# Kernel tuning notes

Measured on AMD Instinct MI355X. Metric: run time of the kernel, lower is better.

Reference implementation:

```python
import jax, jax.numpy as jnp
import numpy as np

B = 8192
HID = [256, 128, 64]
OUT = 5
EPS = 1e-5

# neighbor order for branch i: all other branches in ascending index order
NEIGH = np.array([[j for j in range(8) if j != i] for i in range(8)])  # [8,7]
# adjacency gate (row,col) into A.view(-1,8,8) for branch i, neighbor slot k
# (branch 1 uses a transposed pattern for slots 3..6, exactly as in the source)
_G = [
    [(0,1),(0,2),(0,3),(4,0),(5,0),(6,0),(7,0)],
    [(0,1),(2,1),(3,1),(4,1),(5,1),(6,1),(7,1)],
    [(0,2),(1,2),(3,2),(4,2),(5,2),(6,2),(7,2)],
    [(0,3),(1,3),(2,3),(4,3),(5,3),(6,3),(7,3)],
    [(0,4),(1,4),(2,4),(3,4),(5,4),(6,4),(7,4)],
    [(0,5),(1,5),(2,5),(3,5),(4,5),(6,5),(7,5)],
    [(0,6),(1,6),(2,6),(3,6),(4,6),(5,6),(7,6)],
    [(0,7),(1,7),(2,7),(3,7),(4,7),(5,7),(6,7)],
]
GIDX = np.array([[r * 8 + c for (r, c) in row] for row in _G]).reshape(-1)  # [56]


def setup_inputs() -> dict:
    key = jax.random.key(0)
    ks = iter(jax.random.split(key, 64))
    inp = {}
    inp["state"] = jax.random.normal(next(ks), (B, 3), jnp.float32)
    for i in range(1, 9):
        inp[f"Z{i}"] = jax.random.normal(next(ks), (B, 3), jnp.float32)
    inp["A"] = jax.random.uniform(next(ks), (B, 64), jnp.float32)
    din = 3
    for l, dout in enumerate(HID):
        inp[f"W{l}"] = jax.random.normal(next(ks), (8, din, dout), jnp.float32) * 0.05
        inp[f"b{l}"] = jnp.zeros((8, dout), jnp.float32)
        inp[f"g{l}"] = jnp.ones((8, dout), jnp.float32)
        inp[f"be{l}"] = jnp.zeros((8, dout), jnp.float32)
        inp[f"Wg{l}"] = jax.random.normal(next(ks), (8, 7 * din, 7), jnp.float32) * 0.05
        inp[f"bg{l}"] = jnp.zeros((8, 7), jnp.float32)
        din = dout
    inp["Wout"] = jax.random.normal(next(ks), (8, din, OUT), jnp.float32) * 0.05
    inp["bout"] = jnp.zeros((8, OUT), jnp.float32)
    return inp


def _forward(Z, A, layers, Wout, bout):
    # Z: [B,8,D0], A: [B,64]
    b = Z.shape[0]
    gates = A[:, jnp.asarray(GIDX)].reshape(b, 8, 7)  # [B,8,7]
    neigh = jnp.asarray(NEIGH)
    for (W, bias, g, be, Wg, bg) in layers:
        Zn = Z[:, neigh, :]                                   # [B,8,7,D]
        Zall = Zn.reshape(b, 8, -1)                           # [B,8,7D]
        a = jax.nn.softmax(jnp.einsum('bif,ifo->bio', Zall, Wg) + bg, axis=-1)
        NZ = jnp.einsum('bik,bikd->bid', a * gates, Zn)       # attention-weighted neighbor sum
        h = jnp.einsum('bid,ido->bio', Z + NZ, W) + bias
        mu = h.mean(-1, keepdims=True)
        var = ((h - mu) ** 2).mean(-1, keepdims=True)
        h = (h - mu) / jnp.sqrt(var + EPS) * g + be           # per-branch LayerNorm
        Z = jax.nn.relu(h)
    return jnp.tanh(jnp.einsum('bid,ido->bio', Z, Wout) + bout)  # [B,8,5]


def reference(state, Z1, Z2, Z3, Z4, Z5, Z6, Z7, Z8, A,
              W0, b0, g0, be0, Wg0, bg0,
              W1, b1, g1, be1, Wg1, bg1,
              W2, b2, g2, be2, Wg2, bg2,
              Wout, bout):
    Z = jnp.stack([Z1, Z2, Z3, Z4, Z5, Z6, Z7, Z8], axis=1)  # [B,8,3]
    layers = [(W0, b0, g0, be0, Wg0, bg0),
              (W1, b1, g1, be1, Wg1, bg1),
              (W2, b2, g2, be2, Wg2, bg2)]
    return _forward(Z, A, layers, Wout, bout)
```

## Files before the change

### kernel.cpp

```cpp
#include <hip/hip_runtime.h>
#include <math.h>

typedef _Float16 v8h __attribute__((ext_vector_type(8)));
typedef float    v4f __attribute__((ext_vector_type(4)));

#define NB    32
#define DSTR  264
#define WSTR  68
#define EPSLN 1e-5f

struct KP {
  const float* Z[8];
  const float* A;
  const float *W0, *b0, *g0, *be0, *Wg0, *bg0;
  const float *b1, *g1, *be1, *bg1;
  const float *b2, *g2, *be2, *bg2;
  const float *bout;
  const _Float16 *WgT1, *WgT2, *WT1, *WT2, *WoT, *W0T;
  const float *stats;
  float* out;
};

__device__ __forceinline__ void cvt_one(const float* __restrict__ src, _Float16* __restrict__ dst,
                                        int F, int Osrc, int Opad, int t) {
  const int f  = t % F;
  const int io = t / F;
  const int o  = io % Opad;
  const int i  = io / Opad;
  dst[t] = (o < Osrc) ? (_Float16)src[(i * F + f) * Osrc + o] : (_Float16)0.f;
}

#define E1 114688
#define E2 57344
#define E3 4096
#define E4 262144
#define E5 65536
#define E6 65536
#define NSTAT 136

__global__ void cvt_all(const float* __restrict__ Wg1, const float* __restrict__ Wg2,
                        const float* __restrict__ Wout, const float* __restrict__ W1,
                        const float* __restrict__ W2, const float* __restrict__ W0,
                        const float* __restrict__ b0, _Float16* __restrict__ ws) {
  int t = blockIdx.x * 256 + threadIdx.x;
  if (t < E1) { cvt_one(Wg1, ws, 1792, 7, 8, t); return; }
  t -= E1;
  if (t < E2) { cvt_one(Wg2, ws + E1, 896, 7, 8, t); return; }
  t -= E2;
  if (t < E3) { cvt_one(Wout, ws + E1 + E2, 64, 5, 8, t); return; }
  t -= E3;
  if (t < E4) { cvt_one(W1, ws + E1 + E2 + E3, 256, 128, 128, t); return; }
  t -= E4;
  if (t < E5) { cvt_one(W2, ws + E1 + E2 + E3 + E4, 128, 64, 64, t); return; }
  t -= E5;
  if (t < E6) {
    const int k = t & 31;
    const int o = (t >> 5) & 255;
    const int i = t >> 13;
    ws[E1 + E2 + E3 + E4 + E5 + t] = (k < 3) ? (_Float16)W0[(i * 3 + k) * 256 + o] : (_Float16)0.f;
    return;
  }
  t -= E6;
  if (t < NSTAT * 64) {
    float* sf = (float*)(ws + E1 + E2 + E3 + E4 + E5 + E6);
    const int stat = t >> 6, lane = t & 63;
    const int i = stat / 17, j = stat % 17;
    float v = 0.f;
    #pragma unroll
    for (int c = 0; c < 4; ++c) {
      const int o = lane + c * 64;
      float e;
      if (j < 3)        e = W0[(i * 3 + j) * 256 + o];
      else if (j == 3)  e = b0[i * 256 + o];
      else if (j < 13) {
        const int a = (j - 4) / 3, bb = (j - 4) % 3;
        e = W0[(i * 3 + a) * 256 + o] * W0[(i * 3 + bb) * 256 + o];
      } else if (j < 16) {
        const int d = j - 13;
        e = W0[(i * 3 + d) * 256 + o] * b0[i * 256 + o];
      } else {
        const float x = b0[i * 256 + o]; e = x * x;
      }
      v += e;
    }
    #pragma unroll
    for (int mk = 1; mk < 64; mk <<= 1) v += __shfl_xor(v, mk, 64);
    if (lane == 0) sf[stat] = v * (1.f / 256.f);
  }
}

template<int D, int O, int NPRE>
__device__ __forceinline__ void mfma_layer(
    _Float16* __restrict__ zh, float* __restrict__ wbuf, const float* __restrict__ gbuf,
    const v8h* gpre,
    const _Float16* __restrict__ WgT, const float* __restrict__ bg,
    const _Float16* __restrict__ WT, const float* __restrict__ bias,
    const float* __restrict__ g, const float* __restrict__ be,
    const _Float16* __restrict__ preBase, int preStride, v8h* pre,
    int i, int q, int r)
{
  constexpr int KS = D / 32;
  constexpr int NT = O / 16;

  const _Float16* WgB = WgT + (size_t)(i * 8 + r) * (7 * D) + q * 8;
  const _Float16* WB  = WT  + (size_t)(i * O + r) * D + q * 8;

  v8h dbf[NT];
  #pragma unroll
  for (int n = 0; n < NT; ++n) dbf[n] = *(const v8h*)(WB + (size_t)n * 16 * D);

  v8h gbf[7];
  #pragma unroll
  for (int nb = 0; nb < 7; ++nb) gbf[nb] = gpre[nb];

  v4f ca[2][2];
  #pragma unroll
  for (int mt = 0; mt < 2; ++mt)
    #pragma unroll
    for (int c = 0; c < 2; ++c) ca[mt][c] = (v4f){0.f,0.f,0.f,0.f};

  #pragma unroll
  for (int ks = 0; ks < KS; ++ks) {
    const int d0 = ks * 32 + q * 8;
    v8h gbn[7];
    if (ks + 1 < KS) {
      #pragma unroll
      for (int nb = 0; nb < 7; ++nb)
        gbn[nb] = *(const v8h*)(WgB + nb * D + (ks + 1) * 32);
    }
    #pragma unroll
    for (int nb = 0; nb < 7; ++nb) {
      const int nk = nb + (nb >= i);
      const v8h af0 = *(const v8h*)(zh + (nk * NB + r) * DSTR + d0);
      const v8h af1 = *(const v8h*)(zh + (nk * NB + 16 + r) * DSTR + d0);
      ca[0][nb & 1] = __builtin_amdgcn_mfma_f32_16x16x32_f16(af0, gbf[nb], ca[0][nb & 1], 0, 0, 0);
      ca[1][nb & 1] = __builtin_amdgcn_mfma_f32_16x16x32_f16(af1, gbf[nb], ca[1][nb & 1], 0, 0, 0);
    }
    if (ks + 1 < KS) {
      #pragma unroll
      for (int nb = 0; nb < 7; ++nb) gbf[nb] = gbn[nb];
    }
  }
  const v4f gacc[2] = { ca[0][0] + ca[0][1], ca[1][0] + ca[1][1] };

  const float bgv = (r < 7) ? bg[i * 7 + r] : 0.f;
  #pragma unroll
  for (int mt = 0; mt < 2; ++mt) {
    #pragma unroll
    for (int reg = 0; reg < 4; ++reg) {
      const float v = gacc[mt][reg] + bgv;
      float m = (r < 7) ? v : -3.0e38f;
      #pragma unroll
      for (int mk = 1; mk < 16; mk <<= 1) m = fmaxf(m, __shfl_xor(m, mk, 16));
      const float e = (r < 7) ? __expf(v - m) : 0.f;
      float s = e;
      #pragma unroll
      for (int mk = 1; mk < 16; mk <<= 1) s += __shfl_xor(s, mk, 16);
      const int b = mt * 16 + q * 4 + reg;
      if (r < 7) wbuf[b * WSTR + i * 8 + r] = (e / s) * gbuf[b * WSTR + i * 8 + r];
    }
  }

  v4f acc[2][NT];
  #pragma unroll
  for (int mt = 0; mt < 2; ++mt)
    #pragma unroll
    for (int n = 0; n < NT; ++n) acc[mt][n] = (v4f){0.f,0.f,0.f,0.f};

  _Float16 wh[2][7];
  #pragma unroll
  for (int mt = 0; mt < 2; ++mt)
    #pragma unroll
    for (int nb = 0; nb < 7; ++nb)
      wh[mt][nb] = (_Float16)wbuf[(mt * 16 + r) * WSTR + i * 8 + nb];

  #pragma unroll
  for (int ks = 0; ks < KS; ++ks) {
    const int d0 = ks * 32 + q * 8;
    v8h dbn[NT];
    if (ks + 1 < KS) {
      #pragma unroll
      for (int n = 0; n < NT; ++n)
        dbn[n] = *(const v8h*)(WB + (size_t)n * 16 * D + (ks + 1) * 32);
    }
    v8h x01[2];
    #pragma unroll
    for (int mt = 0; mt < 2; ++mt) {
      v8h zn[7];
      #pragma unroll
      for (int nb = 0; nb < 7; ++nb) {
        const int nk = nb + (nb >= i);
        zn[nb] = *(const v8h*)(zh + ((nk * NB + mt * 16 + r) * DSTR + d0));
      }
      v8h x = *(const v8h*)(zh + ((i * NB + mt * 16 + r) * DSTR + d0));
      x = (x + (zn[0] * wh[mt][0] + zn[1] * wh[mt][1]))
        + ((zn[2] * wh[mt][2] + zn[3] * wh[mt][3])
        + ((zn[4] * wh[mt][4] + zn[5] * wh[mt][5]) + zn[6] * wh[mt][6]));
      x01[mt] = x;
    }
    #pragma unroll
    for (int n = 0; n < NT; ++n) {
      acc[0][n] = __builtin_amdgcn_mfma_f32_16x16x32_f16(x01[0], dbf[n], acc[0][n], 0, 0, 0);
      acc[1][n] = __builtin_amdgcn_mfma_f32_16x16x32_f16(x01[1], dbf[n], acc[1][n], 0, 0, 0);
    }
    if (ks + 1 < KS) {
      #pragma unroll
      for (int n = 0; n < NT; ++n) dbf[n] = dbn[n];
    }
  }

  #pragma unroll
  for (int t = 0; t < NPRE; ++t)
    pre[t] = *(const v8h*)(preBase + (size_t)t * preStride);

  float bv[NT], gv[NT], bev[NT];
  #pragma unroll
  for (int n = 0; n < NT; ++n) {
    const int o = n * 16 + r;
    bv[n] = bias[i * O + o]; gv[n] = g[i * O + o]; bev[n] = be[i * O + o];
  }
  #pragma unroll
  for (int mt = 0; mt < 2; ++mt) {
    #pragma unroll
    for (int reg = 0; reg < 4; ++reg) {
      float s1 = 0.f, s2 = 0.f;
      #pragma unroll
      for (int n = 0; n < NT; ++n) {
        const float h = acc[mt][n][reg] + bv[n];
        acc[mt][n][reg] = h;
        s1 += h; s2 += h * h;
      }
      #pragma unroll
      for (int mk = 1; mk < 16; mk <<= 1) { s1 += __shfl_xor(s1, mk, 16); s2 += __shfl_xor(s2, mk, 16); }
      const float mean = s1 * (1.f / O);
      const float var  = s2 * (1.f / O) - mean * mean;
      const float rs   = rsqrtf(var + EPSLN);
      #pragma unroll
      for (int n = 0; n < NT; ++n) {
        const float h = (acc[mt][n][reg] - mean) * rs * gv[n] + bev[n];
        acc[mt][n][reg] = fmaxf(h, 0.f);
      }
    }
  }
  __syncthreads();
  #pragma unroll
  for (int mt = 0; mt < 2; ++mt)
    #pragma unroll
    for (int n = 0; n < NT; ++n)
      #pragma unroll
      for (int reg = 0; reg < 4; ++reg) {
        const int b = mt * 16 + q * 4 + reg;
        zh[(i * NB + b) * DSTR + n * 16 + r] = (_Float16)acc[mt][n][reg];
      }
  __syncthreads();
}

__launch_bounds__(512, 2)
__global__ void actor_mfma(KP p)
{
  __shared__ __align__(16) _Float16 zh[8 * NB * DSTR];
  __shared__ float wbuf[NB * WSTR];
  __shared__ float gbuf[NB * WSTR];
  __shared__ float xbuf[8 * NB * 4];

  const int i = threadIdx.x >> 6;
  const int u = threadIdx.x & 63;
  const int q = u >> 4, r = u & 15;
  const int bbase = blockIdx.x * NB;

  float w0g[21];
  {
    const int o8c = (u & 7) < 7 ? (u & 7) : 6;
    #pragma unroll
    for (int kd = 0; kd < 21; ++kd) w0g[kd] = p.Wg0[(i * 21 + kd) * 7 + o8c];

    #pragma unroll
    for (int c = 0; c < 2; ++c) {
      const int idx = c * 64 + u;
      if (idx < NB * 3) {
        const int b = idx / 3, d = idx - 3 * (idx / 3);
        zh[(i * NB + b) * DSTR + d] = (_Float16)p.Z[i][(size_t)(bbase + b) * 3 + d];
      }
    }
    for (int t = threadIdx.x; t < NB * 64; t += 512) {
      const int b = t >> 6, ik = t & 63;
      const int ii = ik >> 3, k = ik & 7;
      if (k < 7) {
        const int j = k + (k >= ii);
        const int gidx = (ii == 0 && j <= 3) ? j : 8 * j + ii;
        gbuf[b * WSTR + ik] = p.A[(size_t)(bbase + b) * 64 + gidx];
      }
    }
  }
  __syncthreads();

  {
    const float bgv0 = ((u & 7) < 7) ? p.bg0[i * 7 + (u & 7)] : 0.f;
    for (int c = 0; c < NB / 8; ++c) {
      const int b = c * 8 + (u >> 3), o8 = u & 7;
      float v = -3.0e38f;
      if (o8 < 7) {
        v = bgv0;
        #pragma unroll
        for (int k = 0; k < 7; ++k) {
          const int nk = k + (k >= i);
          const _Float16* zp = zh + (nk * NB + b) * DSTR;
          v += (float)zp[0] * w0g[k * 3 + 0] + (float)zp[1] * w0g[k * 3 + 1]
             + (float)zp[2] * w0g[k * 3 + 2];
        }
      }
      float m = v;
      #pragma unroll
      for (int mk = 1; mk < 8; mk <<= 1) m = fmaxf(m, __shfl_xor(m, mk, 8));
      const float e = (o8 < 7) ? __expf(v - m) : 0.f;
      float s = e;
      #pragma unroll
      for (int mk = 1; mk < 8; mk <<= 1) s += __shfl_xor(s, mk, 8);
      if (o8 < 7) wbuf[b * WSTR + i * 8 + o8] = (e / s) * gbuf[b * WSTR + i * 8 + o8];
    }
  }
  #pragma unroll
  for (int c = 0; c < 2; ++c) {
    const int idx = c * 64 + u;
    if (idx < NB * 3) {
      const int b = idx / 3, d = idx - 3 * (idx / 3);
      float x = (float)zh[(i * NB + b) * DSTR + d];
      #pragma unroll
      for (int k = 0; k < 7; ++k) {
        const int nk = k + (k >= i);
        x += wbuf[b * WSTR + i * 8 + k] * (float)zh[(nk * NB + b) * DSTR + d];
      }
      xbuf[(i * NB + b) * 4 + d] = x;
    }
  }
  v8h gpre1[7];
  {
    const _Float16* gb = p.WgT1 + (size_t)(i * 8 + r) * (7 * 256) + q * 8;
    #pragma unroll
    for (int nb = 0; nb < 7; ++nb) gpre1[nb] = *(const v8h*)(gb + nb * 256);
  }
  float st[17];
  #pragma unroll
  for (int s = 0; s < 17; ++s) st[s] = p.stats[i * 17 + s];
  float b0v[16], g0v[16], be0v[16];
  #pragma unroll
  for (int n = 0; n < 16; ++n) {
    const int o = n * 16 + r;
    b0v[n] = p.b0[i * 256 + o]; g0v[n] = p.g0[i * 256 + o]; be0v[n] = p.be0[i * 256 + o];
  }
  __syncthreads();
  {
    float mu8[8], rs8[8];
    #pragma unroll
    for (int mt = 0; mt < 2; ++mt)
      #pragma unroll
      for (int reg = 0; reg < 4; ++reg) {
        const int row = mt * 16 + q * 4 + reg;
        const float x0 = xbuf[(i * NB + row) * 4 + 0];
        const float x1 = xbuf[(i * NB + row) * 4 + 1];
        const float x2 = xbuf[(i * NB + row) * 4 + 2];
        const float mu = st[3] + x0 * st[0] + x1 * st[1] + x2 * st[2];
        const float ex2 = st[16] + 2.f * (x0 * st[13] + x1 * st[14] + x2 * st[15])
                        + x0 * (x0 * st[4] + 2.f * (x1 * st[5] + x2 * st[6]))
                        + x1 * (x1 * st[8] + 2.f * (x2 * st[9]))
                        + x2 * x2 * st[12];
        mu8[mt * 4 + reg] = mu;
        rs8[mt * 4 + reg] = rsqrtf(fmaxf(ex2 - mu * mu, 0.f) + EPSLN);
      }
    v8h af[2];
    #pragma unroll
    for (int j = 0; j < 8; ++j) { af[0][j] = (_Float16)0.f; af[1][j] = (_Float16)0.f; }
    if (q == 0) {
      #pragma unroll
      for (int mt = 0; mt < 2; ++mt)
        #pragma unroll
        for (int j = 0; j < 3; ++j)
          af[mt][j] = (_Float16)xbuf[(i * NB + mt * 16 + r) * 4 + j];
    }
    const _Float16* WB0 = p.W0T + (size_t)(i * 256 + r) * 32 + q * 8;
    #pragma unroll
    for (int nt = 0; nt < 16; ++nt) {
      const v8h bf = *(const v8h*)(WB0 + (size_t)nt * 16 * 32);
      const float bo = b0v[nt];
      v4f a0 = (v4f){bo, bo, bo, bo}, a1 = a0;
      a0 = __builtin_amdgcn_mfma_f32_16x16x32_f16(af[0], bf, a0, 0, 0, 0);
      a1 = __builtin_amdgcn_mfma_f32_16x16x32_f16(af[1], bf, a1, 0, 0, 0);
      const int o = nt * 16 + r;
      #pragma unroll
      for (int reg = 0; reg < 4; ++reg) {
        const float h0 = (a0[reg] - mu8[reg])     * rs8[reg]     * g0v[nt] + be0v[nt];
        const float h1 = (a1[reg] - mu8[4 + reg]) * rs8[4 + reg] * g0v[nt] + be0v[nt];
        zh[(i * NB + q * 4 + reg) * DSTR + o]      = (_Float16)fmaxf(h0, 0.f);
        zh[(i * NB + 16 + q * 4 + reg) * DSTR + o] = (_Float16)fmaxf(h1, 0.f);
      }
    }
  }
  __syncthreads();

  v8h gpre2[7], wpre[2];
  mfma_layer<256, 128, 7>(zh, wbuf, gbuf, gpre1, p.WgT1, p.bg1, p.WT1, p.b1, p.g1, p.be1,
                          p.WgT2 + (size_t)(i * 8 + r) * (7 * 128) + q * 8, 128, gpre2, i, q, r);
  mfma_layer<128, 64, 2>(zh, wbuf, gbuf, gpre2, p.WgT2, p.bg2, p.WT2, p.b2, p.g2, p.be2,
                         p.WoT + (size_t)(i * 8 + r) * 64 + q * 8, 32, wpre, i, q, r);

  {
    const float bo = (r < 5) ? p.bout[i * 5 + r] : 0.f;
    v4f oacc[2];
    oacc[0] = (v4f){bo, bo, bo, bo}; oacc[1] = oacc[0];
    #pragma unroll
    for (int ks = 0; ks < 2; ++ks) {
      const int d0 = ks * 32 + q * 8;
      const v8h a0 = *(const v8h*)(zh + (i * NB + r) * DSTR + d0);
      const v8h a1 = *(const v8h*)(zh + (i * NB + 16 + r) * DSTR + d0);
      oacc[0] = __builtin_amdgcn_mfma_f32_16x16x32_f16(a0, wpre[ks], oacc[0], 0, 0, 0);
      oacc[1] = __builtin_amdgcn_mfma_f32_16x16x32_f16(a1, wpre[ks], oacc[1], 0, 0, 0);
    }
    if (r < 5) {
      #pragma unroll
      for (int mt = 0; mt < 2; ++mt)
        #pragma unroll
        for (int reg = 0; reg < 4; ++reg) {
          const int b = mt * 16 + q * 4 + reg;
          const float x = oacc[mt][reg];
          const float ex = __expf(2.f * x);
          p.out[((size_t)(bbase + b) * 8 + i) * 5 + r] = 1.f - 2.f / (ex + 1.f);
        }
    }
  }
}

extern "C" void kernel_launch(void* const* d_in, const int* in_sizes, int n_in,
                              void* d_out, int out_size, void* d_ws, size_t ws_size,
                              hipStream_t stream) {
  KP p;
  for (int i = 0; i < 8; ++i) p.Z[i] = (const float*)d_in[1 + i];
  p.A   = (const float*)d_in[9];
  p.W0  = (const float*)d_in[10]; p.b0 = (const float*)d_in[11];
  p.g0  = (const float*)d_in[12]; p.be0 = (const float*)d_in[13];
  p.Wg0 = (const float*)d_in[14]; p.bg0 = (const float*)d_in[15];
  const float* W1  = (const float*)d_in[16]; p.b1 = (const float*)d_in[17];
  p.g1  = (const float*)d_in[18]; p.be1 = (const float*)d_in[19];
  const float* Wg1 = (const float*)d_in[20]; p.bg1 = (const float*)d_in[21];
  const float* W2  = (const float*)d_in[22]; p.b2 = (const float*)d_in[23];
  p.g2  = (const float*)d_in[24]; p.be2 = (const float*)d_in[25];
  const float* Wg2 = (const float*)d_in[26]; p.bg2 = (const float*)d_in[27];
  const float* Wout = (const float*)d_in[28]; p.bout = (const float*)d_in[29];
  p.out = (float*)d_out;

  _Float16* wsH = (_Float16*)d_ws;
  p.WgT1 = wsH;
  p.WgT2 = wsH + E1;
  p.WoT  = wsH + E1 + E2;
  p.WT1  = wsH + E1 + E2 + E3;
  p.WT2  = wsH + E1 + E2 + E3 + E4;
  p.W0T  = wsH + E1 + E2 + E3 + E4 + E5;
  p.stats = (const float*)(wsH + E1 + E2 + E3 + E4 + E5 + E6);

  const int total = E1 + E2 + E3 + E4 + E5 + E6 + NSTAT * 64;
  hipLaunchKernelGGL(cvt_all, dim3((total + 255) / 256), dim3(256), 0, stream,
                     Wg1, Wg2, Wout, W1, W2, p.W0, p.b0, wsH);

  hipLaunchKernelGGL(actor_mfma, dim3(8192 / NB), dim3(512), 0, stream, p);
}
```

Measured before the change: 69.16 us.

## Split each branch's 32-row tile across two waves using 1024-thread blocks

```diff
diff --git a/kernel.cpp b/kernel.cpp
--- a/kernel.cpp
+++ b/kernel.cpp
@@ -97,10 +97,11 @@
     const _Float16* __restrict__ WT, const float* __restrict__ bias,
     const float* __restrict__ g, const float* __restrict__ be,
     const _Float16* __restrict__ preBase, int preStride, v8h* pre,
-    int i, int q, int r)
+    int i, int mt, int q, int r)
 {
   constexpr int KS = D / 32;
   constexpr int NT = O / 16;
+  const int m0 = mt * 16;
 
   const _Float16* WgB = WgT + (size_t)(i * 8 + r) * (7 * D) + q * 8;
   const _Float16* WB  = WT  + (size_t)(i * O + r) * D + q * 8;
@@ -113,12 +114,7 @@
   #pragma unroll
   for (int nb = 0; nb < 7; ++nb) gbf[nb] = gpre[nb];
 
-  v4f ca[2][2];
-  #pragma unroll
-  for (int mt = 0; mt < 2; ++mt)
-    #pragma unroll
-    for (int c = 0; c < 2; ++c) ca[mt][c] = (v4f){0.f,0.f,0.f,0.f};
-
+  v4f ca0 = (v4f){0.f,0.f,0.f,0.f}, ca1 = ca0;
   #pragma unroll
   for (int ks = 0; ks < KS; ++ks) {
     const int d0 = ks * 32 + q * 8;
@@ -131,48 +127,40 @@
     #pragma unroll
     for (int nb = 0; nb < 7; ++nb) {
       const int nk = nb + (nb >= i);
-      const v8h af0 = *(const v8h*)(zh + (nk * NB + r) * DSTR + d0);
-      const v8h af1 = *(const v8h*)(zh + (nk * NB + 16 + r) * DSTR + d0);
-      ca[0][nb & 1] = __builtin_amdgcn_mfma_f32_16x16x32_f16(af0, gbf[nb], ca[0][nb & 1], 0, 0, 0);
-      ca[1][nb & 1] = __builtin_amdgcn_mfma_f32_16x16x32_f16(af1, gbf[nb], ca[1][nb & 1], 0, 0, 0);
+      const v8h af = *(const v8h*)(zh + (nk * NB + m0 + r) * DSTR + d0);
+      if (nb & 1) ca1 = __builtin_amdgcn_mfma_f32_16x16x32_f16(af, gbf[nb], ca1, 0, 0, 0);
+      else        ca0 = __builtin_amdgcn_mfma_f32_16x16x32_f16(af, gbf[nb], ca0, 0, 0, 0);
     }
     if (ks + 1 < KS) {
       #pragma unroll
       for (int nb = 0; nb < 7; ++nb) gbf[nb] = gbn[nb];
     }
   }
-  const v4f gacc[2] = { ca[0][0] + ca[0][1], ca[1][0] + ca[1][1] };
+  const v4f gacc = ca0 + ca1;
 
   const float bgv = (r < 7) ? bg[i * 7 + r] : 0.f;
   #pragma unroll
-  for (int mt = 0; mt < 2; ++mt) {
-    #pragma unroll
-    for (int reg = 0; reg < 4; ++reg) {
-      const float v = gacc[mt][reg] + bgv;
-      float m = (r < 7) ? v : -3.0e38f;
-      #pragma unroll
-      for (int mk = 1; mk < 16; mk <<= 1) m = fmaxf(m, __shfl_xor(m, mk, 16));
-      const float e = (r < 7) ? __expf(v - m) : 0.f;
-      float s = e;
-      #pragma unroll
-      for (int mk = 1; mk < 16; mk <<= 1) s += __shfl_xor(s, mk, 16);
-      const int b = mt * 16 + q * 4 + reg;
-      if (r < 7) wbuf[b * WSTR + i * 8 + r] = (e / s) * gbuf[b * WSTR + i * 8 + r];
-    }
-  }
-
-  v4f acc[2][NT];
-  #pragma unroll
-  for (int mt = 0; mt < 2; ++mt)
-    #pragma unroll
-    for (int n = 0; n < NT; ++n) acc[mt][n] = (v4f){0.f,0.f,0.f,0.f};
-
-  _Float16 wh[2][7];
-  #pragma unroll
-  for (int mt = 0; mt < 2; ++mt)
-    #pragma unroll
-    for (int nb = 0; nb < 7; ++nb)
-      wh[mt][nb] = (_Float16)wbuf[(mt * 16 + r) * WSTR + i * 8 + nb];
+  for (int reg = 0; reg < 4; ++reg) {
+    const float v = gacc[reg] + bgv;
+    float m = (r < 7) ? v : -3.0e38f;
+    #pragma unroll
+    for (int mk = 1; mk < 16; mk <<= 1) m = fmaxf(m, __shfl_xor(m, mk, 16));
+    const float e = (r < 7) ? __expf(v - m) : 0.f;
+    float s = e;
+    #pragma unroll
+    for (int mk = 1; mk < 16; mk <<= 1) s += __shfl_xor(s, mk, 16);
+    const int b = m0 + q * 4 + reg;
+    if (r < 7) wbuf[b * WSTR + i * 8 + r] = (e / s) * gbuf[b * WSTR + i * 8 + r];
+  }
+
+  v4f acc[NT];
+  #pragma unroll
+  for (int n = 0; n < NT; ++n) acc[n] = (v4f){0.f,0.f,0.f,0.f};
+
+  _Float16 wh[7];
+  #pragma unroll
+  for (int nb = 0; nb < 7; ++nb)
+    wh[nb] = (_Float16)wbuf[(m0 + r) * WSTR + i * 8 + nb];
 
   #pragma unroll
   for (int ks = 0; ks < KS; ++ks) {
@@ -183,26 +171,19 @@
       for (int n = 0; n < NT; ++n)
         dbn[n] = *(const v8h*)(WB + (size_t)n * 16 * D + (ks + 1) * 32);
     }
-    v8h x01[2];
-    #pragma unroll
-    for (int mt = 0; mt < 2; ++mt) {
-      v8h zn[7];
-      #pragma unroll
-      for (int nb = 0; nb < 7; ++nb) {
-        const int nk = nb + (nb >= i);
-        zn[nb] = *(const v8h*)(zh + ((nk * NB + mt * 16 + r) * DSTR + d0));
-      }
-      v8h x = *(const v8h*)(zh + ((i * NB + mt * 16 + r) * DSTR + d0));
-      x = (x + (zn[0] * wh[mt][0] + zn[1] * wh[mt][1]))
-        + ((zn[2] * wh[mt][2] + zn[3] * wh[mt][3])
-        + ((zn[4] * wh[mt][4] + zn[5] * wh[mt][5]) + zn[6] * wh[mt][6]));
-      x01[mt] = x;
-    }
-    #pragma unroll
-    for (int n = 0; n < NT; ++n) {
-      acc[0][n] = __builtin_amdgcn_mfma_f32_16x16x32_f16(x01[0], dbf[n], acc[0][n], 0, 0, 0);
-      acc[1][n] = __builtin_amdgcn_mfma_f32_16x16x32_f16(x01[1], dbf[n], acc[1][n], 0, 0, 0);
-    }
+    v8h zn[7];
+    #pragma unroll
+    for (int nb = 0; nb < 7; ++nb) {
+      const int nk = nb + (nb >= i);
+      zn[nb] = *(const v8h*)(zh + ((nk * NB + m0 + r) * DSTR + d0));
+    }
+    v8h x = *(const v8h*)(zh + ((i * NB + m0 + r) * DSTR + d0));
+    x = (x + (zn[0] * wh[0] + zn[1] * wh[1]))
+      + ((zn[2] * wh[2] + zn[3] * wh[3])
+      + ((zn[4] * wh[4] + zn[5] * wh[5]) + zn[6] * wh[6]));
+    #pragma unroll
+    for (int n = 0; n < NT; ++n)
+      acc[n] = __builtin_amdgcn_mfma_f32_16x16x32_f16(x, dbf[n], acc[n], 0, 0, 0);
     if (ks + 1 < KS) {
       #pragma unroll
       for (int n = 0; n < NT; ++n) dbf[n] = dbn[n];
@@ -220,42 +201,37 @@
     bv[n] = bias[i * O + o]; gv[n] = g[i * O + o]; bev[n] = be[i * O + o];
   }
   #pragma unroll
-  for (int mt = 0; mt < 2; ++mt) {
+  for (int reg = 0; reg < 4; ++reg) {
+    float s1 = 0.f, s2 = 0.f;
+    #pragma unroll
+    for (int n = 0; n < NT; ++n) {
+      const float h = acc[n][reg] + bv[n];
+      acc[n][reg] = h;
+      s1 += h; s2 += h * h;
+    }
+    #pragma unroll
+    for (int mk = 1; mk < 16; mk <<= 1) { s1 += __shfl_xor(s1, mk, 16); s2 += __shfl_xor(s2, mk, 16); }
+    const float mean = s1 * (1.f / O);
+    const float var  = s2 * (1.f / O) - mean * mean;
+    const float rs   = rsqrtf(var + EPSLN);
+    #pragma unroll
+    for (int n = 0; n < NT; ++n) {
+      const float h = (acc[n][reg] - mean) * rs * gv[n] + bev[n];
+      acc[n][reg] = fmaxf(h, 0.f);
+    }
+  }
+  __syncthreads();
+  #pragma unroll
+  for (int n = 0; n < NT; ++n)
     #pragma unroll
     for (int reg = 0; reg < 4; ++reg) {
-      float s1 = 0.f, s2 = 0.f;
-      #pragma unroll
-      for (int n = 0; n < NT; ++n) {
-        const float h = acc[mt][n][reg] + bv[n];
-        acc[mt][n][reg] = h;
-        s1 += h; s2 += h * h;
-      }
-      #pragma unroll
-      for (int mk = 1; mk < 16; mk <<= 1) { s1 += __shfl_xor(s1, mk, 16); s2 += __shfl_xor(s2, mk, 16); }
-      const float mean = s1 * (1.f / O);
-      const float var  = s2 * (1.f / O) - mean * mean;
-      const float rs   = rsqrtf(var + EPSLN);
-      #pragma unroll
-      for (int n = 0; n < NT; ++n) {
-        const float h = (acc[mt][n][reg] - mean) * rs * gv[n] + bev[n];
-        acc[mt][n][reg] = fmaxf(h, 0.f);
-      }
-    }
-  }
-  __syncthreads();
-  #pragma unroll
-  for (int mt = 0; mt < 2; ++mt)
-    #pragma unroll
-    for (int n = 0; n < NT; ++n)
-      #pragma unroll
-      for (int reg = 0; reg < 4; ++reg) {
-        const int b = mt * 16 + q * 4 + reg;
-        zh[(i * NB + b) * DSTR + n * 16 + r] = (_Float16)acc[mt][n][reg];
-      }
+      const int b = m0 + q * 4 + reg;
+      zh[(i * NB + b) * DSTR + n * 16 + r] = (_Float16)acc[n][reg];
+    }
   __syncthreads();
 }
 
-__launch_bounds__(512, 2)
+__launch_bounds__(1024)
 __global__ void actor_mfma(KP p)
 {
   __shared__ __align__(16) _Float16 zh[8 * NB * DSTR];
@@ -263,8 +239,11 @@
   __shared__ float gbuf[NB * WSTR];
   __shared__ float xbuf[8 * NB * 4];
 
-  const int i = threadIdx.x >> 6;
-  const int u = threadIdx.x & 63;
+  const int w  = threadIdx.x >> 6;
+  const int i  = w >> 1;
+  const int mt = w & 1;
+  const int m0 = mt * 16;
+  const int u  = threadIdx.x & 63;
   const int q = u >> 4, r = u & 15;
   const int bbase = blockIdx.x * NB;
 
@@ -274,15 +253,14 @@
     #pragma unroll
     for (int kd = 0; kd < 21; ++kd) w0g[kd] = p.Wg0[(i * 21 + kd) * 7 + o8c];
 
-    #pragma unroll
-    for (int c = 0; c < 2; ++c) {
-      const int idx = c * 64 + u;
-      if (idx < NB * 3) {
+    {
+      const int idx = mt * 48 + u;
+      if (u < 48) {
         const int b = idx / 3, d = idx - 3 * (idx / 3);
         zh[(i * NB + b) * DSTR + d] = (_Float16)p.Z[i][(size_t)(bbase + b) * 3 + d];
       }
     }
-    for (int t = threadIdx.x; t < NB * 64; t += 512) {
+    for (int t = threadIdx.x; t < NB * 64; t += 1024) {
       const int b = t >> 6, ik = t & 63;
       const int ii = ik >> 3, k = ik & 7;
       if (k < 7) {
@@ -296,8 +274,8 @@
 
   {
     const float bgv0 = ((u & 7) < 7) ? p.bg0[i * 7 + (u & 7)] : 0.f;
-    for (int c = 0; c < NB / 8; ++c) {
-      const int b = c * 8 + (u >> 3), o8 = u & 7;
+    for (int c = 0; c < 2; ++c) {
+      const int b = m0 + c * 8 + (u >> 3), o8 = u & 7;
       float v = -3.0e38f;
       if (o8 < 7) {
         v = bgv0;
@@ -319,10 +297,9 @@
       if (o8 < 7) wbuf[b * WSTR + i * 8 + o8] = (e / s) * gbuf[b * WSTR + i * 8 + o8];
     }
   }
-  #pragma unroll
-  for (int c = 0; c < 2; ++c) {
-    const int idx = c * 64 + u;
-    if (idx < NB * 3) {
+  {
+    const int idx = mt * 48 + u;
+    if (u < 48) {
       const int b = idx / 3, d = idx - 3 * (idx / 3);
       float x = (float)zh[(i * NB + b) * DSTR + d];
       #pragma unroll
@@ -350,48 +327,41 @@
   }
   __syncthreads();
   {
-    float mu8[8], rs8[8];
-    #pragma unroll
-    for (int mt = 0; mt < 2; ++mt)
-      #pragma unroll
-      for (int reg = 0; reg < 4; ++reg) {
-        const int row = mt * 16 + q * 4 + reg;
-        const float x0 = xbuf[(i * NB + row) * 4 + 0];
-        const float x1 = xbuf[(i * NB + row) * 4 + 1];
-        const float x2 = xbuf[(i * NB + row) * 4 + 2];
-        const float mu = st[3] + x0 * st[0] + x1 * st[1] + x2 * st[2];
-        const float ex2 = st[16] + 2.f * (x0 * st[13] + x1 * st[14] + x2 * st[15])
-                        + x0 * (x0 * st[4] + 2.f * (x1 * st[5] + x2 * st[6]))
-                        + x1 * (x1 * st[8] + 2.f * (x2 * st[9]))
-                        + x2 * x2 * st[12];
-        mu8[mt * 4 + reg] = mu;
-        rs8[mt * 4 + reg] = rsqrtf(fmaxf(ex2 - mu * mu, 0.f) + EPSLN);
-      }
-    v8h af[2];
-    #pragma unroll
-    for (int j = 0; j < 8; ++j) { af[0][j] = (_Float16)0.f; af[1][j] = (_Float16)0.f; }
+    float mu4[4], rs4[4];
+    #pragma unroll
+    for (int reg = 0; reg < 4; ++reg) {
+      const int row = m0 + q * 4 + reg;
+      const float x0 = xbuf[(i * NB + row) * 4 + 0];
+      const float x1 = xbuf[(i * NB + row) * 4 + 1];
+      const float x2 = xbuf[(i * NB + row) * 4 + 2];
+      const float mu = st[3] + x0 * st[0] + x1 * st[1] + x2 * st[2];
+      const float ex2 = st[16] + 2.f * (x0 * st[13] + x1 * st[14] + x2 * st[15])
+                      + x0 * (x0 * st[4] + 2.f * (x1 * st[5] + x2 * st[6]))
+                      + x1 * (x1 * st[8] + 2.f * (x2 * st[9]))
+                      + x2 * x2 * st[12];
+      mu4[reg] = mu;
+      rs4[reg] = rsqrtf(fmaxf(ex2 - mu * mu, 0.f) + EPSLN);
+    }
+    v8h af;
+    #pragma unroll
+    for (int j = 0; j < 8; ++j) af[j] = (_Float16)0.f;
     if (q == 0) {
       #pragma unroll
-      for (int mt = 0; mt < 2; ++mt)
-        #pragma unroll
-        for (int j = 0; j < 3; ++j)
-          af[mt][j] = (_Float16)xbuf[(i * NB + mt * 16 + r) * 4 + j];
+      for (int j = 0; j < 3; ++j)
+        af[j] = (_Float16)xbuf[(i * NB + m0 + r) * 4 + j];
     }
     const _Float16* WB0 = p.W0T + (size_t)(i * 256 + r) * 32 + q * 8;
     #pragma unroll
     for (int nt = 0; nt < 16; ++nt) {
       const v8h bf = *(const v8h*)(WB0 + (size_t)nt * 16 * 32);
       const float bo = b0v[nt];
-      v4f a0 = (v4f){bo, bo, bo, bo}, a1 = a0;
-      a0 = __builtin_amdgcn_mfma_f32_16x16x32_f16(af[0], bf, a0, 0, 0, 0);
-      a1 = __builtin_amdgcn_mfma_f32_16x16x32_f16(af[1], bf, a1, 0, 0, 0);
+      v4f a0 = (v4f){bo, bo, bo, bo};
+      a0 = __builtin_amdgcn_mfma_f32_16x16x32_f16(af, bf, a0, 0, 0, 0);
       const int o = nt * 16 + r;
       #pragma unroll
       for (int reg = 0; reg < 4; ++reg) {
-        const float h0 = (a0[reg] - mu8[reg])     * rs8[reg]     * g0v[nt] + be0v[nt];
-        const float h1 = (a1[reg] - mu8[4 + reg]) * rs8[4 + reg] * g0v[nt] + be0v[nt];
-        zh[(i * NB + q * 4 + reg) * DSTR + o]      = (_Float16)fmaxf(h0, 0.f);
-        zh[(i * NB + 16 + q * 4 + reg) * DSTR + o] = (_Float16)fmaxf(h1, 0.f);
+        const float h0 = (a0[reg] - mu4[reg]) * rs4[reg] * g0v[nt] + be0v[nt];
+        zh[(i * NB + m0 + q * 4 + reg) * DSTR + o] = (_Float16)fmaxf(h0, 0.f);
       }
     }
   }
@@ -399,32 +369,27 @@
 
   v8h gpre2[7], wpre[2];
   mfma_layer<256, 128, 7>(zh, wbuf, gbuf, gpre1, p.WgT1, p.bg1, p.WT1, p.b1, p.g1, p.be1,
-                          p.WgT2 + (size_t)(i * 8 + r) * (7 * 128) + q * 8, 128, gpre2, i, q, r);
+                          p.WgT2 + (size_t)(i * 8 + r) * (7 * 128) + q * 8, 128, gpre2, i, mt, q, r);
   mfma_layer<128, 64, 2>(zh, wbuf, gbuf, gpre2, p.WgT2, p.bg2, p.WT2, p.b2, p.g2, p.be2,
-                         p.WoT + (size_t)(i * 8 + r) * 64 + q * 8, 32, wpre, i, q, r);
+                         p.WoT + (size_t)(i * 8 + r) * 64 + q * 8, 32, wpre, i, mt, q, r);
 
   {
     const float bo = (r < 5) ? p.bout[i * 5 + r] : 0.f;
-    v4f oacc[2];
-    oacc[0] = (v4f){bo, bo, bo, bo}; oacc[1] = oacc[0];
+    v4f oacc = (v4f){bo, bo, bo, bo};
     #pragma unroll
     for (int ks = 0; ks < 2; ++ks) {
       const int d0 = ks * 32 + q * 8;
-      const v8h a0 = *(const v8h*)(zh + (i * NB + r) * DSTR + d0);
-      const v8h a1 = *(const v8h*)(zh + (i * NB + 16 + r) * DSTR + d0);
-      oacc[0] = __builtin_amdgcn_mfma_f32_16x16x32_f16(a0, wpre[ks], oacc[0], 0, 0, 0);
-      oacc[1] = __builtin_amdgcn_mfma_f32_16x16x32_f16(a1, wpre[ks], oacc[1], 0, 0, 0);
+      const v8h a0 = *(const v8h*)(zh + (i * NB + m0 + r) * DSTR + d0);
+      oacc = __builtin_amdgcn_mfma_f32_16x16x32_f16(a0, wpre[ks], oacc, 0, 0, 0);
     }
     if (r < 5) {
       #pragma unroll
-      for (int mt = 0; mt < 2; ++mt)
-        #pragma unroll
-        for (int reg = 0; reg < 4; ++reg) {
-          const int b = mt * 16 + q * 4 + reg;
-          const float x = oacc[mt][reg];
-          const float ex = __expf(2.f * x);
-          p.out[((size_t)(bbase + b) * 8 + i) * 5 + r] = 1.f - 2.f / (ex + 1.f);
-        }
+      for (int reg = 0; reg < 4; ++reg) {
+        const int b = m0 + q * 4 + reg;
+        const float x = oacc[reg];
+        const float ex = __expf(2.f * x);
+        p.out[((size_t)(bbase + b) * 8 + i) * 5 + r] = 1.f - 2.f / (ex + 1.f);
+      }
     }
   }
 }
@@ -460,5 +425,5 @@
   hipLaunchKernelGGL(cvt_all, dim3((total + 255) / 256), dim3(256), 0, stream,
                      Wg1, Wg2, Wout, W1, W2, p.W0, p.b0, wsH);
 
-  hipLaunchKernelGGL(actor_mfma, dim3(8192 / NB), dim3(512), 0, stream, p);
+  hipLaunchKernelGGL(actor_mfma, dim3(8192 / NB), dim3(1024), 0, stream, p);
 }
```

Measured after the change: 110.4 us. +59.7%, slower.
